# Optimization experiments

Hardware: AMD Instinct MI355X
Metric: run time of the kernel (lower is better)

## Reference

```python
import jax, jax.numpy as jnp
import numpy as np

E = 100000   # num entities
D = 300      # embedding dim
R = 1000     # num relations
T = 10000    # aligned pairs
K = 25       # negatives per pair
GAMMA = 1.0


def spmm(rows, cols, vals, x, n_rows):
    # sparse(COO) @ dense: out[r] = sum_{nnz: rows==r} vals * x[cols]
    return jax.ops.segment_sum(vals[:, None] * x[cols], rows, num_segments=n_rows)


def setup_inputs() -> dict:
    key = jax.random.key(0)
    ks = jax.random.split(key, 24)
    g = lambda i, s: jax.random.normal(ks[i], s, dtype=jnp.float32) * 0.05
    ri = lambda i, s, hi: jax.random.randint(ks[i], s, 0, hi, dtype=jnp.int32)
    ru = lambda i, s: jax.random.uniform(ks[i], s, dtype=jnp.float32)
    return {
        'word_embedding': jax.random.normal(ks[0], (E, D), dtype=jnp.float32),
        'kernel_gate': g(1, (D, D)),
        'bias_gate': jnp.zeros((D,), jnp.float32),
        'W1': g(2, (D, D)),
        'W2': g(3, (D, D)),
        'Dense': g(4, (3 * D, D)),
        'Bias': jnp.zeros((D,), jnp.float32),
        'hr_rows': ri(5, (300000,), R), 'hr_cols': ri(6, (300000,), E), 'hr_vals': ru(7, (300000,)),
        'tr_rows': ri(8, (300000,), R), 'tr_cols': ri(9, (300000,), E), 'tr_vals': ru(10, (300000,)),
        'er_rows': ri(11, (300000,), E), 'er_cols': ri(12, (300000,), 2 * R), 'er_vals': ru(13, (300000,)),
        'adj_rows': ri(14, (600000,), E), 'adj_cols': ri(15, (600000,), E), 'adj_vals': ru(16, (600000,)),
        'pos_left': ri(17, (T,), E), 'pos_right': ri(18, (T,), E),
        'neg_right': ri(19, (T, K), E), 'neg_left': ri(20, (T, K), E),
        'mask': jnp.ones((T, K), jnp.float32),
    }


def highway(layer1, layer2, kernel_gate, bias_gate):
    tg = jax.nn.sigmoid(layer1 @ kernel_gate + bias_gate)
    return tg * layer2 + (1.0 - tg) * layer1


def reference(word_embedding, kernel_gate, bias_gate, W1, W2, Dense, Bias,
              hr_rows, hr_cols, hr_vals, tr_rows, tr_cols, tr_vals,
              er_rows, er_cols, er_vals, adj_rows, adj_cols, adj_vals,
              pos_left, pos_right, neg_right, neg_left, mask):
    # L2-normalized frozen word embeddings
    emb = word_embedding / jnp.linalg.norm(word_embedding, axis=-1, keepdims=True)

    # Global relation aggregation (compute_r)
    L = spmm(hr_rows, hr_cols, hr_vals, emb, R)          # [R, D]
    Rm = spmm(tr_rows, tr_cols, tr_vals, emb, R)         # [R, D]
    r_fwd = jnp.concatenate([L, Rm], axis=-1)            # [R, 2D]
    r_emb = jnp.concatenate([r_fwd, -r_fwd], axis=0)     # [2R, 2D]
    nb = spmm(er_rows, er_cols, er_vals, r_emb, E)       # [E, 2D]
    h = jnp.concatenate([emb, nb], axis=-1)              # [E, 3D]
    h = emb + jax.nn.relu(h @ Dense + Bias)

    # Local relation aggregation: 2-layer highway GCN
    gcn1 = jax.nn.relu(spmm(adj_rows, adj_cols, adj_vals, h @ W1, E))
    hg1 = highway(h, gcn1, kernel_gate, bias_gate)
    gcn2 = jax.nn.relu(spmm(adj_rows, adj_cols, adj_vals, hg1 @ W2, E))
    node = highway(hg1, gcn2, kernel_gate, bias_gate)    # [E, D]

    # Hinge alignment loss
    l_x = node[pos_left]                                 # [T, D]
    r_x = node[pos_right]                                # [T, D]
    Dm = jnp.sum(jnp.abs(l_x - r_x), axis=1) + GAMMA     # [T]
    B1 = jnp.sum(jnp.abs(l_x[:, None, :] - node[neg_right]), axis=-1)  # [T, K]
    L1 = jax.nn.relu(Dm[:, None] - B1) * mask
    B2 = jnp.sum(jnp.abs(node[neg_left] - r_x[:, None, :]), axis=-1)   # [T, K]
    L2 = jax.nn.relu(Dm[:, None] - B2) * mask
    return (jnp.sum(L1) + jnp.sum(L2)) / 2.0
```

## Files before the change

kernel.cpp:

```cpp
#include <hip/hip_runtime.h>
#include <math.h>

#define E_N 100000
#define D_N 300
#define R_N 1000
#define T_N 10000
#define K_N 25
#define DP  320
#define BM  64
#define NT  1563

typedef __attribute__((ext_vector_type(8))) short bf16x8;
typedef __attribute__((ext_vector_type(4))) float f32x4;

__device__ __forceinline__ float bf2f(unsigned short h){
  union{ unsigned int u; float f; } c; c.u = ((unsigned int)h)<<16; return c.f;
}
__device__ __forceinline__ unsigned short f2bf(float f){
  union{ float f; unsigned int u; } c; c.f = f;
  unsigned int u = c.u + 0x7FFFu + ((c.u>>16)&1u);
  return (unsigned short)(u>>16);
}
__device__ __forceinline__ unsigned int pack2(float lo, float hi){
  return ((unsigned int)f2bf(hi)<<16) | f2bf(lo);
}

static constexpr size_t BUFB   = (size_t)100032*DP*2;
static constexpr size_t BUFU8  = (size_t)100032*DP;
static constexpr size_t OFF_B0    = 0;
static constexpr size_t OFF_B1    = BUFB;
static constexpr size_t OFF_B2    = 2*BUFB;
static constexpr size_t OFF_B3    = 3*BUFB;
static constexpr size_t OFF_RFWD  = OFF_B3 + BUFU8;
static constexpr size_t OFF_G     = OFF_RFWD + 1310720;
static constexpr size_t OFF_WTKG  = OFF_RFWD + 2400000;
static constexpr size_t OFF_WTW1  = OFF_WTKG + 204800;
static constexpr size_t OFF_WTW2  = OFF_WTW1 + 204800;
static constexpr size_t OFF_WTDN  = OFF_WTW2 + 204800;
static constexpr size_t OFF_WTDN2 = OFF_WTDN + 204800;
static constexpr size_t OFF_BIASP = OFF_WTDN2 + 409600;
static constexpr size_t OFF_BGP   = OFF_BIASP + 1280;
static constexpr size_t OFF_PTRHR = OFF_BGP + 1280;
static constexpr size_t OFF_PTRTR = OFF_PTRHR + 4096;
static constexpr size_t OFF_PTRER = OFF_PTRTR + 4096;
static constexpr size_t OFF_PTRADJ= OFF_PTRER + 400896;
static constexpr size_t OFF_CURHR = OFF_PTRADJ + 400896;
static constexpr size_t OFF_CURTR = OFF_CURHR + 4096;
static constexpr size_t OFF_CURER = OFF_CURTR + 4096;
static constexpr size_t OFF_CURADJ= OFF_CURER + 400896;
static constexpr size_t SZ_CURALL = 4096+4096+400896+400896;
static constexpr size_t OFF_SCHR  = OFF_CURADJ + 400896;
static constexpr size_t OFF_SVHR  = OFF_SCHR + 1200000;
static constexpr size_t OFF_SCTR  = OFF_SVHR + 1200000;
static constexpr size_t OFF_SVTR  = OFF_SCTR + 1200000;
static constexpr size_t OFF_SCER  = OFF_SVTR + 1200000;
static constexpr size_t OFF_SVER  = OFF_SCER + 1200000;
static constexpr size_t OFF_SCADJ = OFF_SVER + 1200000;
static constexpr size_t OFF_SVADJ = OFF_SCADJ + 2400000;
static constexpr size_t OFF_PART  = OFF_SVADJ + 2400000;
static constexpr size_t OFF_BSUM  = OFF_PART + 40000;

__device__ __forceinline__ size_t packIdx(int n, int k, int TK){
  return (size_t)(((n>>4)*TK + (k>>5))<<9) + (((k>>3)&3)<<7) + ((n&15)<<3) + (k&7);
}

__global__ void k_prep_sq(const float* kg, const float* w1, const float* w2,
                          unsigned short* wtKG, unsigned short* wtW1, unsigned short* wtW2){
  int n = blockIdx.x, which = blockIdx.y, k = threadIdx.x;
  const float* src = which==0 ? kg : (which==1 ? w1 : w2);
  unsigned short* dst = which==0 ? wtKG : (which==1 ? wtW1 : wtW2);
  float v = (n < D_N && k < D_N) ? src[k*D_N + n] : 0.f;
  dst[packIdx(n, k, 10)] = f2bf(v);
}

__global__ void k_prep_dense(const float* dn, unsigned short* wt, unsigned short* wt2){
  int n = blockIdx.x, t = threadIdx.x;
  {
    int k = t;
    float v = (n < D_N && k < D_N) ? dn[(size_t)k*D_N + n] : 0.f;
    wt[packIdx(n, k, 10)] = f2bf(v);
  }
  for(int k=t; k<640; k+=320){
    float v = (n < D_N && k < 600) ? dn[(size_t)(300+k)*D_N + n] : 0.f;
    wt2[packIdx(n, k, 20)] = f2bf(v);
  }
}

__global__ void k_prep_bias(const float* bias, const float* bg, float* biasP, float* bgP){
  int t = threadIdx.x;
  biasP[t] = (t < D_N) ? bias[t] : 0.f;
  bgP[t]   = (t < D_N) ? bg[t]   : 0.f;
}

__global__ __launch_bounds__(256) void k_normalize(const float* __restrict__ w,
                                                   unsigned short* __restrict__ embb){
  int wv = threadIdx.x >> 6, lane = threadIdx.x & 63;
  int e = blockIdx.x*4 + wv;
  const float4* row = (const float4*)(w + (size_t)e*D_N);
  float4 x0 = row[lane];
  float4 x1 = make_float4(0.f,0.f,0.f,0.f);
  if(lane < 11) x1 = row[64 + lane];
  float s = x0.x*x0.x + x0.y*x0.y + x0.z*x0.z + x0.w*x0.w
          + x1.x*x1.x + x1.y*x1.y + x1.z*x1.z + x1.w*x1.w;
  #pragma unroll
  for(int off=32; off; off>>=1) s += __shfl_xor(s, off);
  float rn = rsqrtf(s);
  unsigned short* orow = embb + (size_t)e*DP;
  uint2 o0; o0.x = pack2(x0.x*rn, x0.y*rn); o0.y = pack2(x0.z*rn, x0.w*rn);
  *(uint2*)(orow + lane*4) = o0;
  if(lane < 16){
    uint2 o1 = make_uint2(0u,0u);
    if(lane < 11){ o1.x = pack2(x1.x*rn, x1.y*rn); o1.y = pack2(x1.z*rn, x1.w*rn); }
    *(uint2*)(orow + 256 + lane*4) = o1;
  }
}

__global__ void k_count(const int* hr, const int* tr, const int* er, const int* ad,
                        int* cHR, int* cTR, int* cER, int* cAD){
  int i = blockIdx.x*256 + threadIdx.x;
  if(i < 300000)       atomicAdd(&cHR[hr[i]], 1);
  else if(i < 600000)  atomicAdd(&cTR[tr[i-300000]], 1);
  else if(i < 900000)  atomicAdd(&cER[er[i-600000]], 1);
  else if(i < 1500000) atomicAdd(&cAD[ad[i-900000]], 1);
}

__global__ void k_scan_small(int* cHR, int* cTR, int* pHR, int* pTR){
  __shared__ int s[1024];
  int t = threadIdx.x;
  for(int w=0; w<2; w++){
    int* cnt = w ? cTR : cHR; int* ptr = w ? pTR : pHR;
    int c = (t < R_N) ? cnt[t] : 0;
    s[t] = c; __syncthreads();
    for(int off=1; off<1024; off<<=1){
      int v = (t>=off) ? s[t-off] : 0; __syncthreads();
      s[t] += v; __syncthreads();
    }
    int excl = s[t] - c;
    if(t < R_N){ ptr[t] = excl; cnt[t] = excl; }
    if(t == R_N-1) ptr[R_N] = s[t];
    __syncthreads();
  }
}

__global__ void k_scan_part(const int* cER, const int* cAD, int* pER, int* pAD, int* bsum){
  int which = blockIdx.y;
  const int* cnt = which ? cAD : cER;
  int* ptr = which ? pAD : pER;
  __shared__ int s[1024];
  int g = blockIdx.x, t = threadIdx.x, i = g*1024 + t;
  int c = (i < E_N) ? cnt[i] : 0;
  s[t] = c; __syncthreads();
  for(int off=1; off<1024; off<<=1){
    int v = (t>=off) ? s[t-off] : 0; __syncthreads();
    s[t] += v; __syncthreads();
  }
  if(i < E_N) ptr[i] = s[t] - c;
  if(t == 1023) bsum[which*128 + g] = s[1023];
}

__global__ void k_scan_mid(int* bsum, int* pER, int* pAD){
  __shared__ int s[128];
  int t = threadIdx.x;
  for(int w=0; w<2; w++){
    int v = (t < 98) ? bsum[w*128 + t] : 0;
    s[t] = v; __syncthreads();
    for(int off=1; off<128; off<<=1){
      int u = (t>=off) ? s[t-off] : 0; __syncthreads();
      s[t] += u; __syncthreads();
    }
    if(t < 98) bsum[w*128 + t] = s[t] - v;
    if(t == 97){ int* p = w ? pAD : pER; p[E_N] = s[97]; }
    __syncthreads();
  }
}

__global__ void k_scan_add(const int* bsum, int* pER, int* pAD, int* curER, int* curAD){
  int which = blockIdx.y;
  int* ptr = which ? pAD : pER;
  int* cur = which ? curAD : curER;
  int g = blockIdx.x, i = g*1024 + threadIdx.x;
  if(i < E_N){ int v = ptr[i] + bsum[which*128 + g]; ptr[i] = v; cur[i] = v; }
}

__global__ void k_scatter(const int* hr_r, const int* hr_c, const float* hr_v,
                          const int* tr_r, const int* tr_c, const float* tr_v,
                          const int* er_r, const int* er_c, const float* er_v,
                          const int* ad_r, const int* ad_c, const float* ad_v,
                          int* cHR, int* cTR, int* cER, int* cAD,
                          int* scHR, float* svHR, int* scTR, float* svTR,
                          int* scER, float* svER, int* scAD, float* svAD){
  int i = blockIdx.x*256 + threadIdx.x;
  if(i < 300000){ int p=atomicAdd(&cHR[hr_r[i]],1); scHR[p]=hr_c[i]; svHR[p]=hr_v[i]; }
  else if(i < 600000){ int j=i-300000; int p=atomicAdd(&cTR[tr_r[j]],1); scTR[p]=tr_c[j]; svTR[p]=tr_v[j]; }
  else if(i < 900000){ int j=i-600000; int p=atomicAdd(&cER[er_r[j]],1); scER[p]=er_c[j]; svER[p]=er_v[j]; }
  else if(i < 1500000){ int j=i-900000; int p=atomicAdd(&cAD[ad_r[j]],1); scAD[p]=ad_c[j]; svAD[p]=ad_v[j]; }
}

__global__ __launch_bounds__(256) void k_spmm_rel(
    const int* __restrict__ ptr, const int* __restrict__ scol, const float* __restrict__ sval,
    const unsigned short* __restrict__ embb, unsigned short* __restrict__ rfwdb, int off){
  int w = threadIdx.x >> 6, lane = threadIdx.x & 63;
  int r = blockIdx.x*2 + (w>>1);
  int half = w & 1;
  int elem = half*160 + 4*lane;
  bool act = (lane < 40) && (elem < 300);
  int b = ptr[r], e2 = ptr[r+1];
  float a0=0.f, a1=0.f, a2=0.f, a3=0.f;
  if(act){
    const unsigned short* base = embb + elem;
    int j = b;
    for(; j+4 <= e2; j += 4){
      int c0=scol[j], c1=scol[j+1], c2=scol[j+2], c3=scol[j+3];
      float v0=sval[j], v1=sval[j+1], v2=sval[j+2], v3=sval[j+3];
      uint2 x0 = *(const uint2*)(base + (size_t)c0*DP);
      uint2 x1 = *(const uint2*)(base + (size_t)c1*DP);
      uint2 x2 = *(const uint2*)(base + (size_t)c2*DP);
      uint2 x3 = *(const uint2*)(base + (size_t)c3*DP);
      a0 += v0*bf2f(x0.x&0xFFFF) + v1*bf2f(x1.x&0xFFFF) + v2*bf2f(x2.x&0xFFFF) + v3*bf2f(x3.x&0xFFFF);
      a1 += v0*bf2f(x0.x>>16)    + v1*bf2f(x1.x>>16)    + v2*bf2f(x2.x>>16)    + v3*bf2f(x3.x>>16);
      a2 += v0*bf2f(x0.y&0xFFFF) + v1*bf2f(x1.y&0xFFFF) + v2*bf2f(x2.y&0xFFFF) + v3*bf2f(x3.y&0xFFFF);
      a3 += v0*bf2f(x0.y>>16)    + v1*bf2f(x1.y>>16)    + v2*bf2f(x2.y>>16)    + v3*bf2f(x3.y>>16);
    }
    for(; j < e2; j++){
      int c = scol[j]; float v = sval[j];
      uint2 x = *(const uint2*)(base + (size_t)c*DP);
      a0 += v*bf2f(x.x&0xFFFF); a1 += v*bf2f(x.x>>16);
      a2 += v*bf2f(x.y&0xFFFF); a3 += v*bf2f(x.y>>16);
    }
    uint2 o;
    o.x = pack2(a0, a1);
    o.y = pack2(a2, a3);
    *(uint2*)&rfwdb[(size_t)r*640 + off + elem] = o;
  }
}

__global__ __launch_bounds__(256) void k_gemm_G(const unsigned short* __restrict__ rfwdb,
    const unsigned short* __restrict__ Bt2, unsigned short* __restrict__ G){
  __shared__ unsigned short bufG[64][640];
  int tid = threadIdx.x;
  int wave = tid>>6, lane = tid&63, quad = lane>>4, l16 = lane&15;
  int m0 = blockIdx.x * 64;
  #pragma unroll
  for(int i=0; i<20; i++){
    int idx = tid + i*256;
    int row = idx/80, colc = idx%80;
    *(uint4*)&bufG[row][(colc ^ (row&7))*8] = *(const uint4*)(rfwdb + (size_t)(m0+row)*640 + colc*8);
  }
  __syncthreads();
  f32x4 acc[4][5];
  #pragma unroll
  for(int mf=0; mf<4; mf++)
    #pragma unroll
    for(int nf=0; nf<5; nf++) acc[mf][nf] = (f32x4){0.f,0.f,0.f,0.f};
  #pragma unroll 2
  for(int kk=0; kk<640; kk+=32){
    bf16x8 af[4], bfr[5];
    #pragma unroll
    for(int mf=0; mf<4; mf++)
      af[mf] = *(const bf16x8*)&bufG[mf*16 + l16][(((kk>>3)+quad) ^ (l16&7))*8];
    #pragma unroll
    for(int nf=0; nf<5; nf++)
      bfr[nf] = *(const bf16x8*)(Bt2 + ((size_t)(((wave*5+nf)*20 + (kk>>5))<<6) + lane)*8);
    #pragma unroll
    for(int mf=0; mf<4; mf++)
      #pragma unroll
      for(int nf=0; nf<5; nf++)
        acc[mf][nf] = __builtin_amdgcn_mfma_f32_16x16x32_bf16(af[mf], bfr[nf], acc[mf][nf], 0, 0, 0);
  }
  __syncthreads();
  unsigned short (*ob)[DP] = (unsigned short(*)[DP])bufG;
  #pragma unroll
  for(int mf=0; mf<4; mf++)
    #pragma unroll
    for(int nf=0; nf<5; nf++){
      int col = wave*80 + nf*16 + l16;
      #pragma unroll
      for(int i=0; i<4; i++){
        int rowl = mf*16 + quad*4 + i;
        ob[rowl][((col>>3) ^ (rowl&7))*8 + (col&7)] = f2bf(acc[mf][nf][i]);
      }
    }
  __syncthreads();
  #pragma unroll
  for(int i=0; i<10; i++){
    int idx = tid + i*256;
    int row = idx/40, colc = idx%40;
    *(uint4*)(G + (size_t)(m0+row)*DP + colc*8) = *(const uint4*)&ob[row][(colc ^ (row&7))*8];
  }
}

__global__ __launch_bounds__(256) void k_er_g(
    const int* __restrict__ ptr, const int* __restrict__ scol, const float* __restrict__ sval,
    const unsigned short* __restrict__ G, unsigned short* __restrict__ nb){
  int w = threadIdx.x >> 6, lane = threadIdx.x & 63;
  int e = blockIdx.x*4 + w;
  int b = ptr[e], en = ptr[e+1];
  if(lane < 40){
    float a0[8], a1[8];
    #pragma unroll
    for(int i=0;i<8;i++){ a0[i]=0.f; a1[i]=0.f; }
    const unsigned short* gb = G + lane*8;
    int j = b;
    for(; j+2 <= en; j += 2){
      int c0=scol[j], c1=scol[j+1];
      float v0=sval[j], v1=sval[j+1];
      int p0=c0, p1=c1;
      if(c0 >= R_N){ p0 = c0-R_N; v0 = -v0; }
      if(c1 >= R_N){ p1 = c1-R_N; v1 = -v1; }
      bf16x8 x0 = *(const bf16x8*)(gb + (size_t)p0*DP);
      bf16x8 x1 = *(const bf16x8*)(gb + (size_t)p1*DP);
      #pragma unroll
      for(int i=0;i<8;i++){ a0[i] += v0*bf2f((unsigned short)x0[i]);
                            a1[i] += v1*bf2f((unsigned short)x1[i]); }
    }
    if(j < en){
      int c=scol[j]; float v=sval[j];
      int p=c; if(c >= R_N){ p = c-R_N; v = -v; }
      bf16x8 x = *(const bf16x8*)(gb + (size_t)p*DP);
      #pragma unroll
      for(int i=0;i<8;i++) a0[i] += v*bf2f((unsigned short)x[i]);
    }
    bf16x8 o;
    #pragma unroll
    for(int i=0;i<8;i++) o[i] = (short)f2bf(a0[i]+a1[i]);
    *(bf16x8*)&nb[(size_t)e*DP + lane*8] = o;
  }
}

__global__ __launch_bounds__(256) void k_spmm_hw(
    const int* __restrict__ ptr, const int* __restrict__ scol, const float* __restrict__ sval,
    const unsigned short* __restrict__ hw, const unsigned char* __restrict__ tg,
    const unsigned short* __restrict__ res, unsigned short* __restrict__ out){
  int w = threadIdx.x >> 6, lane = threadIdx.x & 63;
  int e = blockIdx.x*4 + w;
  int b = ptr[e], en = ptr[e+1];
  if(lane < 40){
    float a0[8], a1[8];
    #pragma unroll
    for(int i=0;i<8;i++){ a0[i]=0.f; a1[i]=0.f; }
    const unsigned short* base = hw + lane*8;
    int j = b;
    for(; j+2 <= en; j += 2){
      int c0 = scol[j], c1 = scol[j+1];
      float v0 = sval[j], v1 = sval[j+1];
      bf16x8 x0 = *(const bf16x8*)(base + (size_t)c0*DP);
      bf16x8 x1 = *(const bf16x8*)(base + (size_t)c1*DP);
      #pragma unroll
      for(int i=0;i<8;i++){ a0[i] += v0 * bf2f((unsigned short)x0[i]);
                            a1[i] += v1 * bf2f((unsigned short)x1[i]); }
    }
    if(j < en){
      int c = scol[j]; float v = sval[j];
      bf16x8 x = *(const bf16x8*)(base + (size_t)c*DP);
      #pragma unroll
      for(int i=0;i<8;i++) a0[i] += v * bf2f((unsigned short)x[i]);
    }
    uint2 tu = *(const uint2*)(tg + (size_t)e*DP + lane*8);
    bf16x8 rv = *(const bf16x8*)(res + (size_t)e*DP + lane*8);
    bf16x8 o;
    #pragma unroll
    for(int i=0;i<8;i++){
      unsigned int word = (i<4) ? tu.x : tu.y;
      float g = (float)((word >> ((i&3)*8)) & 255u);
      g = (g + 0.5f) * 0.00390625f;
      float gcn = fmaxf(a0[i]+a1[i], 0.f);
      o[i] = (short)f2bf(g*gcn + (1.f-g)*bf2f(rv[i]));
    }
    *(bf16x8*)&out[(size_t)e*DP + lane*8] = o;
  }
}

__device__ __forceinline__ void stageA(unsigned short (*buf)[DP],
                                       const unsigned short* __restrict__ src, int tid){
  #pragma unroll
  for(int i=0; i<10; i++){
    int idx = tid + i*256;
    int row = idx/40, colc = idx%40;
    *(uint4*)&buf[row][(colc ^ (row&7))*8] = *(const uint4*)(src + (size_t)idx*8);
  }
}
__device__ __forceinline__ void storeT(unsigned short* dst,
                                       const unsigned short (*buf)[DP], int tid){
  #pragma unroll
  for(int i=0; i<10; i++){
    int idx = tid + i*256;
    int row = idx/40, colc = idx%40;
    *(uint4*)(dst + (size_t)idx*8) = *(const uint4*)&buf[row][(colc ^ (row&7))*8];
  }
}
__device__ __forceinline__ void storeT16(unsigned short* __restrict__ dst,
                                         const unsigned short (*buf)[DP], int tid){
  #pragma unroll
  for(int i=0; i<3; i++){
    int idx = tid + i*256;
    if(idx < 640){
      int row = idx/40, colc = idx%40;
      *(uint4*)(dst + (size_t)idx*8) = *(const uint4*)&buf[row][(colc ^ (row&7))*8];
    }
  }
}
__device__ __forceinline__ void kloop(f32x4 acc[4][5], const unsigned short (*As)[DP],
    const unsigned short* __restrict__ Bt, int TK, int tkb, int wave, int quad, int l16){
  int lane = (quad<<4) | l16;
  #pragma unroll 2
  for(int kk=0; kk<DP; kk+=32){
    bf16x8 af[4], bfr[5];
    #pragma unroll
    for(int mf=0; mf<4; mf++)
      af[mf] = *(const bf16x8*)&As[mf*16 + l16][(((kk>>3)+quad) ^ (l16&7))*8];
    #pragma unroll
    for(int nf=0; nf<5; nf++)
      bfr[nf] = *(const bf16x8*)(Bt + ((size_t)(((wave*5+nf)*TK + tkb + (kk>>5))<<6) + lane)*8);
    #pragma unroll
    for(int mf=0; mf<4; mf++)
      #pragma unroll
      for(int nf=0; nf<5; nf++)
        acc[mf][nf] = __builtin_amdgcn_mfma_f32_16x16x32_bf16(af[mf], bfr[nf], acc[mf][nf], 0, 0, 0);
  }
}

__global__ __launch_bounds__(256,3) void k_gemm_f(
    const unsigned short* __restrict__ Ain,
    const unsigned short* __restrict__ BtD,
    const unsigned short* nbG,
    const float* __restrict__ biasP,
    const unsigned short* __restrict__ BtW,
    const unsigned short* __restrict__ BtG,
    const float* __restrict__ bgP,
    unsigned short* hOut,
    unsigned short* __restrict__ hwOut,
    unsigned char*  __restrict__ tgOut,
    int dense){
  __shared__ unsigned short buf[BM][DP];
  __shared__ unsigned short scr[16][DP];
  int tid = threadIdx.x;
  int wave = tid>>6, lane = tid&63, quad = lane>>4, l16 = lane&15;
  int m0 = blockIdx.x * BM;

  stageA(buf, Ain + (size_t)m0*DP, tid);
  __syncthreads();

  if(dense){
    float breg[5];
    #pragma unroll
    for(int nf=0; nf<5; nf++) breg[nf] = biasP[wave*80 + nf*16 + l16];
    f32x4 acc[4][5];
    #pragma unroll
    for(int mf=0; mf<4; mf++)
      #pragma unroll
      for(int nf=0; nf<5; nf++) acc[mf][nf] = (f32x4){0.f,0.f,0.f,0.f};
    kloop(acc, buf, BtD, 10, 0, wave, quad, l16);
    const unsigned short* nbrow = nbG + (size_t)m0*DP;
    #pragma unroll
    for(int mf=0; mf<4; mf++){
      #pragma unroll
      for(int i=0; i<3; i++){
        int idx = tid + i*256;
        if(idx < 640){
          int row = idx/40, colc = idx%40;
          *(uint4*)&scr[row][(colc ^ (row&7))*8] =
              *(const uint4*)(nbrow + (size_t)(mf*16+row)*DP + colc*8);
        }
      }
      __syncthreads();
      #pragma unroll
      for(int nf=0; nf<5; nf++){
        int col = wave*80 + nf*16 + l16;
        #pragma unroll
        for(int i=0; i<4; i++){
          int rowl = mf*16 + quad*4 + i;
          int rloc = quad*4 + i;
          int a = ((col>>3) ^ (rowl&7))*8 + (col&7);
          float nbv  = bf2f(scr[rloc][((col>>3) ^ (rloc&7))*8 + (col&7)]);
          float resv = bf2f(buf[rowl][a]);
          buf[rowl][a] = f2bf(resv + fmaxf(acc[mf][nf][i] + breg[nf] + nbv, 0.f));
        }
      }
      __syncthreads();
    }
    storeT(hOut + (size_t)m0*DP, buf, tid);
  }

  {
    f32x4 acc[4][5];
    #pragma unroll
    for(int mf=0; mf<4; mf++)
      #pragma unroll
      for(int nf=0; nf<5; nf++) acc[mf][nf] = (f32x4){0.f,0.f,0.f,0.f};
    kloop(acc, buf, BtW, 10, 0, wave, quad, l16);
    #pragma unroll
    for(int mf=0; mf<4; mf++){
      #pragma unroll
      for(int nf=0; nf<5; nf++){
        int col = wave*80 + nf*16 + l16;
        #pragma unroll
        for(int i=0; i<4; i++){
          int rowl = quad*4 + i;
          scr[rowl][((col>>3) ^ (rowl&7))*8 + (col&7)] = f2bf(acc[mf][nf][i]);
        }
      }
      __syncthreads();
      storeT16(hwOut + (size_t)(m0 + mf*16)*DP, scr, tid);
      __syncthreads();
    }
  }

  {
    float greg[5];
    #pragma unroll
    for(int nf=0; nf<5; nf++) greg[nf] = bgP[wave*80 + nf*16 + l16];
    f32x4 acc[4][5];
    #pragma unroll
    for(int mf=0; mf<4; mf++)
      #pragma unroll
      for(int nf=0; nf<5; nf++) acc[mf][nf] = (f32x4){0.f,0.f,0.f,0.f};
    kloop(acc, buf, BtG, 10, 0, wave, quad, l16);
    unsigned char* bu = (unsigned char*)scr;
    #pragma unroll
    for(int c=0; c<2; c++){
      #pragma unroll
      for(int mh=0; mh<2; mh++){
        int mf = c*2 + mh;
        #pragma unroll
        for(int nf=0; nf<5; nf++){
          int col = wave*80 + nf*16 + l16;
          #pragma unroll
          for(int i=0; i<4; i++){
            int rowl = mh*16 + quad*4 + i;
            float tg = 1.f / (1.f + expf(-(acc[mf][nf][i] + greg[nf])));
            int u = (int)(tg * 256.f);
            u = u < 0 ? 0 : (u > 255 ? 255 : u);
            bu[rowl*DP + col] = (unsigned char)u;
          }
        }
      }
      __syncthreads();
      unsigned char* dst = tgOut + (size_t)(m0 + c*32)*DP;
      #pragma unroll
      for(int i=0; i<3; i++){
        int idx = tid + i*256;
        if(idx < 640) *(uint4*)(dst + (size_t)idx*16) = *(const uint4*)(bu + (size_t)idx*16);
      }
      __syncthreads();
    }
  }
}

__global__ __launch_bounds__(256) void k_loss(const unsigned short* __restrict__ node,
                       const int* __restrict__ pl, const int* __restrict__ pr,
                       const int* __restrict__ nr, const int* __restrict__ nl,
                       const float* __restrict__ mask,
                       float* __restrict__ part){
  int t = blockIdx.x;
  int w = threadIdx.x >> 6, lane = threadIdx.x & 63;
  __shared__ float wsum[4];
  bool act = lane < 40;
  size_t lb = (size_t)pl[t]*DP, rb = (size_t)pr[t]*DP;
  float lv[8], rv[8];
  #pragma unroll
  for(int i=0;i<8;i++){ lv[i]=0.f; rv[i]=0.f; }
  if(act){
    bf16x8 L = *(const bf16x8*)&node[lb + lane*8];
    bf16x8 R = *(const bf16x8*)&node[rb + lane*8];
    #pragma unroll
    for(int i=0;i<8;i++){ lv[i]=bf2f((unsigned short)L[i]); rv[i]=bf2f((unsigned short)R[i]); }
  }
  float s = 0.f;
  #pragma unroll
  for(int i=0;i<8;i++) s += fabsf(lv[i] - rv[i]);
  #pragma unroll
  for(int off=32; off; off>>=1) s += __shfl_xor(s, off);
  float dm = s + 1.0f;

  float local = 0.f;
  for(int k=w; k<K_N; k+=8){
    int k2 = k + 4;
    bool h2 = k2 < K_N;
    int kb = h2 ? k2 : k;
    float s1a=0.f, s2a=0.f, s1b=0.f, s2b=0.f;
    if(act){
      size_t nrb  = (size_t)nr[t*K_N+k ]*DP, nlb  = (size_t)nl[t*K_N+k ]*DP;
      size_t nrb2 = (size_t)nr[t*K_N+kb]*DP, nlb2 = (size_t)nl[t*K_N+kb]*DP;
      bf16x8 X1 = *(const bf16x8*)&node[nrb  + lane*8];
      bf16x8 Y1 = *(const bf16x8*)&node[nlb  + lane*8];
      bf16x8 X2 = *(const bf16x8*)&node[nrb2 + lane*8];
      bf16x8 Y2 = *(const bf16x8*)&node[nlb2 + lane*8];
      #pragma unroll
      for(int i=0;i<8;i++){
        s1a += fabsf(lv[i] - bf2f((unsigned short)X1[i]));
        s2a += fabsf(bf2f((unsigned short)Y1[i]) - rv[i]);
        s1b += fabsf(lv[i] - bf2f((unsigned short)X2[i]));
        s2b += fabsf(bf2f((unsigned short)Y2[i]) - rv[i]);
      }
    }
    #pragma unroll
    for(int off=32; off; off>>=1){
      s1a += __shfl_xor(s1a, off); s2a += __shfl_xor(s2a, off);
      s1b += __shfl_xor(s1b, off); s2b += __shfl_xor(s2b, off);
    }
    if(lane==0){
      local += (fmaxf(dm - s1a, 0.f) + fmaxf(dm - s2a, 0.f)) * mask[t*K_N+k];
      if(h2) local += (fmaxf(dm - s1b, 0.f) + fmaxf(dm - s2b, 0.f)) * mask[t*K_N+k2];
    }
  }
  if(lane==0) wsum[w] = local;
  __syncthreads();
  if(threadIdx.x==0) part[t] = wsum[0]+wsum[1]+wsum[2]+wsum[3];
}

__global__ void k_reduce(const float* part, float* out){
  __shared__ float s[256];
  int t = threadIdx.x;
  float a = 0.f;
  for(int i=t; i<T_N; i+=256) a += part[i];
  s[t] = a; __syncthreads();
  for(int off=128; off; off>>=1){ if(t<off) s[t]+=s[t+off]; __syncthreads(); }
  if(t==0) out[0] = s[0]*0.5f;
}

extern "C" void kernel_launch(void* const* d_in, const int* in_sizes, int n_in,
                              void* d_out, int out_size, void* d_ws, size_t ws_size,
                              hipStream_t stream){
  const float* Wemb = (const float*)d_in[0];
  const float* KG   = (const float*)d_in[1];
  const float* BG   = (const float*)d_in[2];
  const float* W1   = (const float*)d_in[3];
  const float* W2   = (const float*)d_in[4];
  const float* DN   = (const float*)d_in[5];
  const float* BI   = (const float*)d_in[6];
  const int* HRr = (const int*)d_in[7];  const int* HRc = (const int*)d_in[8];  const float* HRv = (const float*)d_in[9];
  const int* TRr = (const int*)d_in[10]; const int* TRc = (const int*)d_in[11]; const float* TRv = (const float*)d_in[12];
  const int* ERr = (const int*)d_in[13]; const int* ERc = (const int*)d_in[14]; const float* ERv = (const float*)d_in[15];
  const int* ADr = (const int*)d_in[16]; const int* ADc = (const int*)d_in[17]; const float* ADv = (const float*)d_in[18];
  const int* PL = (const int*)d_in[19]; const int* PR = (const int*)d_in[20];
  const int* NR = (const int*)d_in[21]; const int* NL = (const int*)d_in[22];
  const float* MASK = (const float*)d_in[23];
  char* ws = (char*)d_ws;

  unsigned short* B0 = (unsigned short*)(ws + OFF_B0);
  unsigned short* B1 = (unsigned short*)(ws + OFF_B1);
  unsigned short* B2 = (unsigned short*)(ws + OFF_B2);
  unsigned char*  B3 = (unsigned char*)(ws + OFF_B3);
  unsigned short* rfwdb = (unsigned short*)(ws + OFF_RFWD);
  unsigned short* Gb    = (unsigned short*)(ws + OFF_G);
  unsigned short* wtKG = (unsigned short*)(ws + OFF_WTKG);
  unsigned short* wtW1 = (unsigned short*)(ws + OFF_WTW1);
  unsigned short* wtW2 = (unsigned short*)(ws + OFF_WTW2);
  unsigned short* wtDN = (unsigned short*)(ws + OFF_WTDN);
  unsigned short* wtDN2= (unsigned short*)(ws + OFF_WTDN2);
  float* biasP = (float*)(ws + OFF_BIASP);
  float* bgP   = (float*)(ws + OFF_BGP);
  int* pHR = (int*)(ws + OFF_PTRHR); int* pTR = (int*)(ws + OFF_PTRTR);
  int* pER = (int*)(ws + OFF_PTRER); int* pAD = (int*)(ws + OFF_PTRADJ);
  int* cHR = (int*)(ws + OFF_CURHR); int* cTR = (int*)(ws + OFF_CURTR);
  int* cER = (int*)(ws + OFF_CURER); int* cAD = (int*)(ws + OFF_CURADJ);
  int* scHR = (int*)(ws + OFF_SCHR); float* svHR = (float*)(ws + OFF_SVHR);
  int* scTR = (int*)(ws + OFF_SCTR); float* svTR = (float*)(ws + OFF_SVTR);
  int* scER = (int*)(ws + OFF_SCER); float* svER = (float*)(ws + OFF_SVER);
  int* scAD = (int*)(ws + OFF_SCADJ); float* svAD = (float*)(ws + OFF_SVADJ);
  float* part = (float*)(ws + OFF_PART);
  int* bsum   = (int*)(ws + OFF_BSUM);

  (void)hipMemsetAsync(ws + OFF_CURHR, 0, SZ_CURALL, stream);
  (void)hipMemsetAsync(ws + OFF_RFWD, 0, 1310720, stream);

  k_prep_sq<<<dim3(320,3), 320, 0, stream>>>(KG, W1, W2, wtKG, wtW1, wtW2);
  k_prep_dense<<<320, 320, 0, stream>>>(DN, wtDN, wtDN2);
  k_prep_bias<<<1, 320, 0, stream>>>(BI, BG, biasP, bgP);
  k_normalize<<<E_N/4, 256, 0, stream>>>(Wemb, B0);

  k_count<<<5860, 256, 0, stream>>>(HRr, TRr, ERr, ADr, cHR, cTR, cER, cAD);
  k_scan_small<<<1, 1024, 0, stream>>>(cHR, cTR, pHR, pTR);
  k_scan_part<<<dim3(98,2), 1024, 0, stream>>>(cER, cAD, pER, pAD, bsum);
  k_scan_mid<<<1, 128, 0, stream>>>(bsum, pER, pAD);
  k_scan_add<<<dim3(98,2), 1024, 0, stream>>>(bsum, pER, pAD, cER, cAD);
  k_scatter<<<5860, 256, 0, stream>>>(HRr,HRc,HRv, TRr,TRc,TRv, ERr,ERc,ERv, ADr,ADc,ADv,
                                      cHR,cTR,cER,cAD, scHR,svHR, scTR,svTR, scER,svER, scAD,svAD);

  k_spmm_rel<<<R_N/2, 256, 0, stream>>>(pHR, scHR, svHR, B0, rfwdb, 0);
  k_spmm_rel<<<R_N/2, 256, 0, stream>>>(pTR, scTR, svTR, B0, rfwdb, 300);

  k_gemm_G<<<16, 256, 0, stream>>>(rfwdb, wtDN2, Gb);
  k_er_g<<<E_N/4, 256, 0, stream>>>(pER, scER, svER, Gb, B1);

  k_gemm_f<<<NT, 256, 0, stream>>>(B0, wtDN, B1, biasP,
                                   wtW1, wtKG, bgP, B1, B2, B3, 1);
  k_spmm_hw<<<E_N/4, 256, 0, stream>>>(pAD, scAD, svAD, B2, B3, B1, B0);
  k_gemm_f<<<NT, 256, 0, stream>>>(B0, nullptr, nullptr, nullptr,
                                   wtW2, wtKG, bgP, nullptr, B2, B3, 0);
  k_spmm_hw<<<E_N/4, 256, 0, stream>>>(pAD, scAD, svAD, B2, B3, B0, B1);

  k_loss<<<T_N, 256, 0, stream>>>(B1, PL, PR, NR, NL, MASK, part);
  k_reduce<<<1, 256, 0, stream>>>(part, (float*)d_out);
}
```

Measured before the change: 1.130 ms.

## Interleave CSR col/val pairs and partition count/scatter by row range

Column indices and values of each sparse matrix are now stored interleaved as uint2 pairs, so each SpMM kernel fetches an entry with one 8-byte load instead of two separate loads. The count and scatter kernels launch 8x as many blocks, each handling only the rows in one eighth of the row range. This keeps atomics and scatter writes within a narrower address window, which should improve cache locality. The cost is that every input row index is now read 8 times.

```diff
diff --git a/kernel.cpp b/kernel.cpp
--- a/kernel.cpp
+++ b/kernel.cpp
@@ -49,15 +49,11 @@
 static constexpr size_t OFF_CURER = OFF_CURTR + 4096;
 static constexpr size_t OFF_CURADJ= OFF_CURER + 400896;
 static constexpr size_t SZ_CURALL = 4096+4096+400896+400896;
-static constexpr size_t OFF_SCHR  = OFF_CURADJ + 400896;
-static constexpr size_t OFF_SVHR  = OFF_SCHR + 1200000;
-static constexpr size_t OFF_SCTR  = OFF_SVHR + 1200000;
-static constexpr size_t OFF_SVTR  = OFF_SCTR + 1200000;
-static constexpr size_t OFF_SCER  = OFF_SVTR + 1200000;
-static constexpr size_t OFF_SVER  = OFF_SCER + 1200000;
-static constexpr size_t OFF_SCADJ = OFF_SVER + 1200000;
-static constexpr size_t OFF_SVADJ = OFF_SCADJ + 2400000;
-static constexpr size_t OFF_PART  = OFF_SVADJ + 2400000;
+static constexpr size_t OFF_SPHR  = OFF_CURADJ + 400896;
+static constexpr size_t OFF_SPTR  = OFF_SPHR + 2400000;
+static constexpr size_t OFF_SPER  = OFF_SPTR + 2400000;
+static constexpr size_t OFF_SPAD  = OFF_SPER + 2400000;
+static constexpr size_t OFF_PART  = OFF_SPAD + 4800000;
 static constexpr size_t OFF_BSUM  = OFF_PART + 40000;
 
 __device__ __forceinline__ size_t packIdx(int n, int k, int TK){
@@ -117,11 +113,22 @@
 
 __global__ void k_count(const int* hr, const int* tr, const int* er, const int* ad,
                         int* cHR, int* cTR, int* cER, int* cAD){
-  int i = blockIdx.x*256 + threadIdx.x;
-  if(i < 300000)       atomicAdd(&cHR[hr[i]], 1);
-  else if(i < 600000)  atomicAdd(&cTR[tr[i-300000]], 1);
-  else if(i < 900000)  atomicAdd(&cER[er[i-600000]], 1);
-  else if(i < 1500000) atomicAdd(&cAD[ad[i-900000]], 1);
+  int g = blockIdx.x & 7;
+  int i = (blockIdx.x >> 3)*256 + threadIdx.x;
+  unsigned loR = g*125u, loE = g*12500u;
+  if(i < 300000){
+    int r = hr[i];
+    if((unsigned)(r-loR) < 125u) atomicAdd(&cHR[r], 1);
+  } else if(i < 600000){
+    int r = tr[i-300000];
+    if((unsigned)(r-loR) < 125u) atomicAdd(&cTR[r], 1);
+  } else if(i < 900000){
+    int r = er[i-600000];
+    if((unsigned)(r-loE) < 12500u) atomicAdd(&cER[r], 1);
+  } else if(i < 1500000){
+    int r = ad[i-900000];
+    if((unsigned)(r-loE) < 12500u) atomicAdd(&cAD[r], 1);
+  }
 }
 
 __global__ void k_scan_small(int* cHR, int* cTR, int* pHR, int* pTR){
@@ -187,17 +194,39 @@
                           const int* er_r, const int* er_c, const float* er_v,
                           const int* ad_r, const int* ad_c, const float* ad_v,
                           int* cHR, int* cTR, int* cER, int* cAD,
-                          int* scHR, float* svHR, int* scTR, float* svTR,
-                          int* scER, float* svER, int* scAD, float* svAD){
-  int i = blockIdx.x*256 + threadIdx.x;
-  if(i < 300000){ int p=atomicAdd(&cHR[hr_r[i]],1); scHR[p]=hr_c[i]; svHR[p]=hr_v[i]; }
-  else if(i < 600000){ int j=i-300000; int p=atomicAdd(&cTR[tr_r[j]],1); scTR[p]=tr_c[j]; svTR[p]=tr_v[j]; }
-  else if(i < 900000){ int j=i-600000; int p=atomicAdd(&cER[er_r[j]],1); scER[p]=er_c[j]; svER[p]=er_v[j]; }
-  else if(i < 1500000){ int j=i-900000; int p=atomicAdd(&cAD[ad_r[j]],1); scAD[p]=ad_c[j]; svAD[p]=ad_v[j]; }
+                          uint2* spHR, uint2* spTR, uint2* spER, uint2* spAD){
+  int g = blockIdx.x & 7;
+  int i = (blockIdx.x >> 3)*256 + threadIdx.x;
+  unsigned loR = g*125u, loE = g*12500u;
+  if(i < 300000){
+    int r = hr_r[i];
+    if((unsigned)(r-loR) < 125u){
+      int p = atomicAdd(&cHR[r],1);
+      spHR[p] = make_uint2((unsigned)hr_c[i], __float_as_uint(hr_v[i]));
+    }
+  } else if(i < 600000){
+    int j = i-300000; int r = tr_r[j];
+    if((unsigned)(r-loR) < 125u){
+      int p = atomicAdd(&cTR[r],1);
+      spTR[p] = make_uint2((unsigned)tr_c[j], __float_as_uint(tr_v[j]));
+    }
+  } else if(i < 900000){
+    int j = i-600000; int r = er_r[j];
+    if((unsigned)(r-loE) < 12500u){
+      int p = atomicAdd(&cER[r],1);
+      spER[p] = make_uint2((unsigned)er_c[j], __float_as_uint(er_v[j]));
+    }
+  } else if(i < 1500000){
+    int j = i-900000; int r = ad_r[j];
+    if((unsigned)(r-loE) < 12500u){
+      int p = atomicAdd(&cAD[r],1);
+      spAD[p] = make_uint2((unsigned)ad_c[j], __float_as_uint(ad_v[j]));
+    }
+  }
 }
 
 __global__ __launch_bounds__(256) void k_spmm_rel(
-    const int* __restrict__ ptr, const int* __restrict__ scol, const float* __restrict__ sval,
+    const int* __restrict__ ptr, const uint2* __restrict__ sp,
     const unsigned short* __restrict__ embb, unsigned short* __restrict__ rfwdb, int off){
   int w = threadIdx.x >> 6, lane = threadIdx.x & 63;
   int r = blockIdx.x*2 + (w>>1);
@@ -210,8 +239,10 @@
     const unsigned short* base = embb + elem;
     int j = b;
     for(; j+4 <= e2; j += 4){
-      int c0=scol[j], c1=scol[j+1], c2=scol[j+2], c3=scol[j+3];
-      float v0=sval[j], v1=sval[j+1], v2=sval[j+2], v3=sval[j+3];
+      uint2 q0=sp[j], q1=sp[j+1], q2=sp[j+2], q3=sp[j+3];
+      int c0=(int)q0.x, c1=(int)q1.x, c2=(int)q2.x, c3=(int)q3.x;
+      float v0=__uint_as_float(q0.y), v1=__uint_as_float(q1.y),
+            v2=__uint_as_float(q2.y), v3=__uint_as_float(q3.y);
       uint2 x0 = *(const uint2*)(base + (size_t)c0*DP);
       uint2 x1 = *(const uint2*)(base + (size_t)c1*DP);
       uint2 x2 = *(const uint2*)(base + (size_t)c2*DP);
@@ -222,7 +253,8 @@
       a3 += v0*bf2f(x0.y>>16)    + v1*bf2f(x1.y>>16)    + v2*bf2f(x2.y>>16)    + v3*bf2f(x3.y>>16);
     }
     for(; j < e2; j++){
-      int c = scol[j]; float v = sval[j];
+      uint2 q = sp[j];
+      int c = (int)q.x; float v = __uint_as_float(q.y);
       uint2 x = *(const uint2*)(base + (size_t)c*DP);
       a0 += v*bf2f(x.x&0xFFFF); a1 += v*bf2f(x.x>>16);
       a2 += v*bf2f(x.y&0xFFFF); a3 += v*bf2f(x.y>>16);
@@ -290,7 +322,7 @@
 }
 
 __global__ __launch_bounds__(256) void k_er_g(
-    const int* __restrict__ ptr, const int* __restrict__ scol, const float* __restrict__ sval,
+    const int* __restrict__ ptr, const uint2* __restrict__ sp,
     const unsigned short* __restrict__ G, unsigned short* __restrict__ nb){
   int w = threadIdx.x >> 6, lane = threadIdx.x & 63;
   int e = blockIdx.x*4 + w;
@@ -302,8 +334,9 @@
     const unsigned short* gb = G + lane*8;
     int j = b;
     for(; j+2 <= en; j += 2){
-      int c0=scol[j], c1=scol[j+1];
-      float v0=sval[j], v1=sval[j+1];
+      uint2 q0=sp[j], q1=sp[j+1];
+      int c0=(int)q0.x, c1=(int)q1.x;
+      float v0=__uint_as_float(q0.y), v1=__uint_as_float(q1.y);
       int p0=c0, p1=c1;
       if(c0 >= R_N){ p0 = c0-R_N; v0 = -v0; }
       if(c1 >= R_N){ p1 = c1-R_N; v1 = -v1; }
@@ -314,7 +347,8 @@
                             a1[i] += v1*bf2f((unsigned short)x1[i]); }
     }
     if(j < en){
-      int c=scol[j]; float v=sval[j];
+      uint2 q = sp[j];
+      int c=(int)q.x; float v=__uint_as_float(q.y);
       int p=c; if(c >= R_N){ p = c-R_N; v = -v; }
       bf16x8 x = *(const bf16x8*)(gb + (size_t)p*DP);
       #pragma unroll
@@ -328,7 +362,7 @@
 }
 
 __global__ __launch_bounds__(256) void k_spmm_hw(
-    const int* __restrict__ ptr, const int* __restrict__ scol, const float* __restrict__ sval,
+    const int* __restrict__ ptr, const uint2* __restrict__ sp,
     const unsigned short* __restrict__ hw, const unsigned char* __restrict__ tg,
     const unsigned short* __restrict__ res, unsigned short* __restrict__ out){
   int w = threadIdx.x >> 6, lane = threadIdx.x & 63;
@@ -341,8 +375,9 @@
     const unsigned short* base = hw + lane*8;
     int j = b;
     for(; j+2 <= en; j += 2){
-      int c0 = scol[j], c1 = scol[j+1];
-      float v0 = sval[j], v1 = sval[j+1];
+      uint2 q0=sp[j], q1=sp[j+1];
+      int c0=(int)q0.x, c1=(int)q1.x;
+      float v0=__uint_as_float(q0.y), v1=__uint_as_float(q1.y);
       bf16x8 x0 = *(const bf16x8*)(base + (size_t)c0*DP);
       bf16x8 x1 = *(const bf16x8*)(base + (size_t)c1*DP);
       #pragma unroll
@@ -350,7 +385,8 @@
                             a1[i] += v1 * bf2f((unsigned short)x1[i]); }
     }
     if(j < en){
-      int c = scol[j]; float v = sval[j];
+      uint2 q = sp[j];
+      int c = (int)q.x; float v = __uint_as_float(q.y);
       bf16x8 x = *(const bf16x8*)(base + (size_t)c*DP);
       #pragma unroll
       for(int i=0;i<8;i++) a0[i] += v * bf2f((unsigned short)x[i]);
@@ -654,10 +690,10 @@
   int* pER = (int*)(ws + OFF_PTRER); int* pAD = (int*)(ws + OFF_PTRADJ);
   int* cHR = (int*)(ws + OFF_CURHR); int* cTR = (int*)(ws + OFF_CURTR);
   int* cER = (int*)(ws + OFF_CURER); int* cAD = (int*)(ws + OFF_CURADJ);
-  int* scHR = (int*)(ws + OFF_SCHR); float* svHR = (float*)(ws + OFF_SVHR);
-  int* scTR = (int*)(ws + OFF_SCTR); float* svTR = (float*)(ws + OFF_SVTR);
-  int* scER = (int*)(ws + OFF_SCER); float* svER = (float*)(ws + OFF_SVER);
-  int* scAD = (int*)(ws + OFF_SCADJ); float* svAD = (float*)(ws + OFF_SVADJ);
+  uint2* spHR = (uint2*)(ws + OFF_SPHR);
+  uint2* spTR = (uint2*)(ws + OFF_SPTR);
+  uint2* spER = (uint2*)(ws + OFF_SPER);
+  uint2* spAD = (uint2*)(ws + OFF_SPAD);
   float* part = (float*)(ws + OFF_PART);
   int* bsum   = (int*)(ws + OFF_BSUM);
 
@@ -669,26 +705,26 @@
   k_prep_bias<<<1, 320, 0, stream>>>(BI, BG, biasP, bgP);
   k_normalize<<<E_N/4, 256, 0, stream>>>(Wemb, B0);
 
-  k_count<<<5860, 256, 0, stream>>>(HRr, TRr, ERr, ADr, cHR, cTR, cER, cAD);
+  k_count<<<5860*8, 256, 0, stream>>>(HRr, TRr, ERr, ADr, cHR, cTR, cER, cAD);
   k_scan_small<<<1, 1024, 0, stream>>>(cHR, cTR, pHR, pTR);
   k_scan_part<<<dim3(98,2), 1024, 0, stream>>>(cER, cAD, pER, pAD, bsum);
   k_scan_mid<<<1, 128, 0, stream>>>(bsum, pER, pAD);
   k_scan_add<<<dim3(98,2), 1024, 0, stream>>>(bsum, pER, pAD, cER, cAD);
-  k_scatter<<<5860, 256, 0, stream>>>(HRr,HRc,HRv, TRr,TRc,TRv, ERr,ERc,ERv, ADr,ADc,ADv,
-                                      cHR,cTR,cER,cAD, scHR,svHR, scTR,svTR, scER,svER, scAD,svAD);
-
-  k_spmm_rel<<<R_N/2, 256, 0, stream>>>(pHR, scHR, svHR, B0, rfwdb, 0);
-  k_spmm_rel<<<R_N/2, 256, 0, stream>>>(pTR, scTR, svTR, B0, rfwdb, 300);
+  k_scatter<<<5860*8, 256, 0, stream>>>(HRr,HRc,HRv, TRr,TRc,TRv, ERr,ERc,ERv, ADr,ADc,ADv,
+                                        cHR,cTR,cER,cAD, spHR, spTR, spER, spAD);
+
+  k_spmm_rel<<<R_N/2, 256, 0, stream>>>(pHR, spHR, B0, rfwdb, 0);
+  k_spmm_rel<<<R_N/2, 256, 0, stream>>>(pTR, spTR, B0, rfwdb, 300);
 
   k_gemm_G<<<16, 256, 0, stream>>>(rfwdb, wtDN2, Gb);
-  k_er_g<<<E_N/4, 256, 0, stream>>>(pER, scER, svER, Gb, B1);
+  k_er_g<<<E_N/4, 256, 0, stream>>>(pER, spER, Gb, B1);
 
   k_gemm_f<<<NT, 256, 0, stream>>>(B0, wtDN, B1, biasP,
                                    wtW1, wtKG, bgP, B1, B2, B3, 1);
-  k_spmm_hw<<<E_N/4, 256, 0, stream>>>(pAD, scAD, svAD, B2, B3, B1, B0);
+  k_spmm_hw<<<E_N/4, 256, 0, stream>>>(pAD, spAD, B2, B3, B1, B0);
   k_gemm_f<<<NT, 256, 0, stream>>>(B0, nullptr, nullptr, nullptr,
                                    wtW2, wtKG, bgP, nullptr, B2, B3, 0);
-  k_spmm_hw<<<E_N/4, 256, 0, stream>>>(pAD, scAD, svAD, B2, B3, B0, B1);
+  k_spmm_hw<<<E_N/4, 256, 0, stream>>>(pAD, spAD, B2, B3, B0, B1);
 
   k_loss<<<T_N, 256, 0, stream>>>(B1, PL, PR, NR, NL, MASK, part);
   k_reduce<<<1, 256, 0, stream>>>(part, (float*)d_out);
```

Result: slower. 1.226 ms (+8.5%).
